# Kernel optimization log

Hardware: AMD Instinct MI355X
Metric: run time of the kernel (lower is better)

## Reference

```python
import jax, jax.numpy as jnp
import numpy as np

N = 3072
E = 32 * N
H = 8
IN_F = 64
OUT_F = 16
ALPHA = 0.2  # LeakyReLU slope
NEG_INF = -9e15


def setup_inputs() -> dict:
    key = jax.random.key(0)
    k1, k2, k3, k4, k5 = jax.random.split(key, 5)
    h = jax.random.normal(k1, (N, IN_F), dtype=jnp.float32)
    edge_index = jax.random.randint(k2, (2, E), 0, N, dtype=jnp.int64)
    S = jax.random.uniform(k3, (N, N), dtype=jnp.float32)
    W = jax.random.normal(k4, (H, IN_F, OUT_F), dtype=jnp.float32) * 0.2
    a = jax.random.normal(k5, (H, 2 * OUT_F, 1), dtype=jnp.float32) * 0.3
    raw_gamma = jnp.ones((H,), dtype=jnp.float32)
    return {"h": h, "edge_index": edge_index, "S": S, "W": W, "a": a, "raw_gamma": raw_gamma}


def reference(h, edge_index, S, W, a, raw_gamma):
    n = h.shape[0]
    # dense adjacency from edge list (to_dense_adj semantics: adj[src, dst] += 1)
    adj = jnp.zeros((n, n), dtype=h.dtype).at[edge_index[0], edge_index[1]].add(1.0)
    # per-head projection: Wh [H, N, O]
    Wh = jnp.einsum('nf,hfo->hno', h, W)
    o = W.shape[2]
    a1 = a[:, :o, 0]  # [H, O]
    a2 = a[:, o:, 0]  # [H, O]
    e1 = jnp.einsum('hno,ho->hn', Wh, a1)  # Wh @ a[:O]
    e2 = jnp.einsum('hno,ho->hn', Wh, a2)  # Wh @ a[O:]
    e = jax.nn.leaky_relu(e1[:, :, None] + e2[:, None, :], ALPHA)  # [H, N, N]
    att = jnp.where(adj[None] > 0, e, jnp.asarray(NEG_INF, e.dtype))
    gamma = jax.nn.softplus(raw_gamma)  # [H], non-negative gate
    att = att * (1.0 + gamma[:, None, None] * S[None])
    att = jax.nn.softmax(att, axis=-1)  # row softmax (dim=1 of [N, N])
    # dropout is identity in eval mode
    h_prime = jnp.einsum('hnm,hmo->hno', att, Wh)  # [H, N, O]
    h_prime = jax.nn.elu(h_prime)  # concat=True per head
    # concat heads along feature dim -> [N, H*O]
    return jnp.transpose(h_prime, (1, 0, 2)).reshape(n, -1)
```

## Files before the change

kernel.cpp:

```cpp
#include <hip/hip_runtime.h>
#include <math.h>

#define N_NODES 3072
#define H_HEADS 8
#define IN_FEAT 64
#define OUT_FEAT 16
#define WORDS_PER_ROW 96
#define MAXD 256
#define SCATTER_BLOCKS 384
#define WH_NPB 16
#define WH_BLOCKS (N_NODES / WH_NPB)

__launch_bounds__(256)
__global__ void scatter_and_wh_kernel(const int* __restrict__ ei, int E,
                                      unsigned int* __restrict__ bits,
                                      const float* __restrict__ hfeat,
                                      const float* __restrict__ W,
                                      const float* __restrict__ a,
                                      float* __restrict__ Wh,
                                      float* __restrict__ e1,
                                      float* __restrict__ e2) {
    __shared__ __align__(16) float Wt[H_HEADS][OUT_FEAT][68];
    __shared__ __align__(16) float hs[WH_NPB][IN_FEAT];

    int tid = threadIdx.x;
    if (blockIdx.x < SCATTER_BLOCKS) {
        int e = blockIdx.x * 256 + tid;
        if (e < E) {
            int r = ei[e];
            int c = ei[E + e];
            atomicOr(&bits[r * WORDS_PER_ROW + (c >> 5)], 1u << (c & 31));
        }
        return;
    }

    int node_base = (blockIdx.x - SCATTER_BLOCKS) * WH_NPB;
    for (int idx = tid; idx < H_HEADS * IN_FEAT * OUT_FEAT; idx += 256) {
        int hh = idx >> 10, f = (idx >> 4) & 63, o = idx & 15;
        Wt[hh][o][f] = W[idx];
    }
    for (int idx = tid; idx < WH_NPB * IN_FEAT; idx += 256)
        hs[idx >> 6][idx & 63] = hfeat[node_base * IN_FEAT + idx];
    __syncthreads();

    int ng = tid >> 7;
    int hh = (tid >> 4) & 7;
    int o  = tid & 15;
    float a1v = a[hh * 2 * OUT_FEAT + o];
    float a2v = a[hh * 2 * OUT_FEAT + OUT_FEAT + o];

    float4 w[16];
#pragma unroll
    for (int q = 0; q < 16; ++q)
        w[q] = *(const float4*)&Wt[hh][o][4 * q];

    for (int n = ng; n < WH_NPB; n += 2) {
        float acc = 0.f;
#pragma unroll
        for (int q = 0; q < 16; ++q) {
            float4 hv = *(const float4*)&hs[n][4 * q];
            acc = fmaf(hv.x, w[q].x, acc);
            acc = fmaf(hv.y, w[q].y, acc);
            acc = fmaf(hv.z, w[q].z, acc);
            acc = fmaf(hv.w, w[q].w, acc);
        }
        int node = node_base + n;
        Wh[(hh * N_NODES + node) * OUT_FEAT + o] = acc;
        float p1 = acc * a1v, p2 = acc * a2v;
#pragma unroll
        for (int m = 1; m < 16; m <<= 1) {
            p1 += __shfl_xor(p1, m, 64);
            p2 += __shfl_xor(p2, m, 64);
        }
        if (o == 0) {
            e1[hh * N_NODES + node] = p1;
            e2[hh * N_NODES + node] = p2;
        }
    }
}

__launch_bounds__(256)
__global__ void gat_main_kernel(const unsigned int* __restrict__ bits,
                                const float* __restrict__ S,
                                const float* __restrict__ Wh,
                                const float* __restrict__ e1,
                                const float* __restrict__ e2,
                                const float* __restrict__ raw_gamma,
                                float* __restrict__ out) {
    __shared__ int lds_j[MAXD];
    __shared__ float lds_s[MAXD];
    __shared__ float lds_p[H_HEADS][MAXD];
    __shared__ int lds_cnt;
    __shared__ int fb_j;
    int i = blockIdx.x;
    int tid = threadIdx.x;
    int wave = tid >> 6, lane = tid & 63;

    if (wave == 0) {
        unsigned int w0 = bits[i * WORDS_PER_ROW + lane];
        unsigned int w1 = (lane < WORDS_PER_ROW - 64) ? bits[i * WORDS_PER_ROW + 64 + lane] : 0u;
        int c = __popc(w0) + __popc(w1);
        int s = c;
#pragma unroll
        for (int d = 1; d < 64; d <<= 1) {
            int v = __shfl_up(s, d, 64);
            if (lane >= d) s += v;
        }
        int off = s - c;
        if (lane == 63) lds_cnt = s;
        unsigned int b = w0;
        int base = lane << 5;
        while (b) {
            int bit = __ffs(b) - 1; b &= b - 1;
            if (off < MAXD) {
                int j = base + bit;
                lds_j[off] = j;
                lds_s[off] = S[i * N_NODES + j];
            }
            ++off;
        }
        b = w1; base = (64 + lane) << 5;
        while (b) {
            int bit = __ffs(b) - 1; b &= b - 1;
            if (off < MAXD) {
                int j = base + bit;
                lds_j[off] = j;
                lds_s[off] = S[i * N_NODES + j];
            }
            ++off;
        }
    }
    __syncthreads();
    int cnt = lds_cnt;
    if (cnt > MAXD) cnt = MAXD;

    if (cnt == 0) {
        if (wave == 0) {
            float bm = 3.4e38f; int bj = 0;
            for (int j = lane; j < N_NODES; j += 64) {
                float sv = S[i * N_NODES + j];
                if (sv < bm) { bm = sv; bj = j; }
            }
            for (int m = 1; m < 64; m <<= 1) {
                float bm2 = __shfl_xor(bm, m, 64);
                int bj2 = __shfl_xor(bj, m, 64);
                if (bm2 < bm || (bm2 == bm && bj2 < bj)) { bm = bm2; bj = bj2; }
            }
            if (lane == 0) fb_j = bj;
        }
        __syncthreads();
        int jj = fb_j;
        if (tid < H_HEADS * OUT_FEAT) {
            int hh = tid >> 4, o = tid & 15;
            float x = Wh[(hh * N_NODES + jj) * OUT_FEAT + o];
            out[i * (H_HEADS * OUT_FEAT) + hh * OUT_FEAT + o] =
                x > 0.f ? x : __expf(x) - 1.f;
        }
        return;
    }

    int half = lane >> 5;
    int hl = lane & 31;
    int hh = wave * 2 + half;
    float g = log1pf(__expf(raw_gamma[hh]));
    float e1v = e1[hh * N_NODES + i];
    float l = 0.f;
    for (int k = hl; k < cnt; k += 32) {
        int j = lds_j[k];
        float x = e1v + e2[hh * N_NODES + j];
        x = x > 0.f ? x : 0.2f * x;
        float p = __expf(x * (1.f + g * lds_s[k]));
        lds_p[hh][k] = p;
        l += p;
    }
#pragma unroll
    for (int m = 1; m < 32; m <<= 1)
        l += __shfl_xor(l, m, 64);

    int kgrp = hl >> 4, o = hl & 15;
    float acc = 0.f;
    for (int kk = kgrp; kk < cnt; kk += 2)
        acc = fmaf(lds_p[hh][kk], Wh[(hh * N_NODES + lds_j[kk]) * OUT_FEAT + o], acc);
    acc += __shfl_xor(acc, 16, 64);
    if (kgrp == 0) {
        float x = acc / l;
        out[i * (H_HEADS * OUT_FEAT) + hh * OUT_FEAT + o] =
            x > 0.f ? x : __expf(x) - 1.f;
    }
}

extern "C" void kernel_launch(void* const* d_in, const int* in_sizes, int n_in,
                              void* d_out, int out_size, void* d_ws, size_t ws_size,
                              hipStream_t stream) {
    const float* hfeat = (const float*)d_in[0];
    const int* ei      = (const int*)d_in[1];
    const float* S     = (const float*)d_in[2];
    const float* W     = (const float*)d_in[3];
    const float* a     = (const float*)d_in[4];
    const float* rg    = (const float*)d_in[5];
    float* out = (float*)d_out;

    char* ws = (char*)d_ws;
    unsigned int* bits = (unsigned int*)ws;
    float* Wh = (float*)(ws + 1179648);
    float* e1 = (float*)(ws + 1179648 + 1572864);
    float* e2 = e1 + H_HEADS * N_NODES;

    int nbits = N_NODES * WORDS_PER_ROW;
    hipMemsetAsync(bits, 0, (size_t)nbits * 4, stream);

    int E = in_sizes[1] / 2;
    scatter_and_wh_kernel<<<SCATTER_BLOCKS + WH_BLOCKS, 256, 0, stream>>>(
        ei, E, bits, hfeat, W, a, Wh, e1, e2);

    gat_main_kernel<<<N_NODES, 256, 0, stream>>>(bits, S, Wh, e1, e2, rg, out);
}
```

Measured before the change: 112.6 us.

## Replace adjacency bitmap with capped per-row neighbor lists and LDS-staged e2

Instead of setting bits in a dense N×N bitmap, the scatter kernel now appends each destination to a per-row list with a capacity of 96, using an atomic counter per row. The main kernel reads these lists directly, so the wave-0 popcount, prefix-scan and bit-extraction pass goes away, and only a 12 KB count array needs clearing instead of a 1.2 MB bitmap. Since lists can hold the same neighbor twice, an O(deg²) check in LDS marks duplicates so they get zero weight. The e1/e2 arrays are stored node-major so each neighbor's eight per-head e2 values load as two float4 and are staged in LDS. The tradeoffs are a silent truncation if any row has more than 96 edges, and a neighbor order that varies between runs.

```diff
diff --git a/kernel.cpp b/kernel.cpp
--- a/kernel.cpp
+++ b/kernel.cpp
@@ -5,21 +5,21 @@
 #define H_HEADS 8
 #define IN_FEAT 64
 #define OUT_FEAT 16
-#define WORDS_PER_ROW 96
-#define MAXD 256
+#define MAXD 96
 #define SCATTER_BLOCKS 384
 #define WH_NPB 16
 #define WH_BLOCKS (N_NODES / WH_NPB)
 
 __launch_bounds__(256)
 __global__ void scatter_and_wh_kernel(const int* __restrict__ ei, int E,
-                                      unsigned int* __restrict__ bits,
+                                      int* __restrict__ cnt,
+                                      int* __restrict__ adj,
                                       const float* __restrict__ hfeat,
                                       const float* __restrict__ W,
                                       const float* __restrict__ a,
                                       float* __restrict__ Wh,
-                                      float* __restrict__ e1,
-                                      float* __restrict__ e2) {
+                                      float* __restrict__ e1t,
+                                      float* __restrict__ e2t) {
     __shared__ __align__(16) float Wt[H_HEADS][OUT_FEAT][68];
     __shared__ __align__(16) float hs[WH_NPB][IN_FEAT];
 
@@ -29,7 +29,8 @@
         if (e < E) {
             int r = ei[e];
             int c = ei[E + e];
-            atomicOr(&bits[r * WORDS_PER_ROW + (c >> 5)], 1u << (c & 31));
+            int pos = atomicAdd(&cnt[r], 1);
+            if (pos < MAXD) adj[r * MAXD + pos] = c;
         }
         return;
     }
@@ -73,66 +74,46 @@
             p2 += __shfl_xor(p2, m, 64);
         }
         if (o == 0) {
-            e1[hh * N_NODES + node] = p1;
-            e2[hh * N_NODES + node] = p2;
+            e1t[node * H_HEADS + hh] = p1;
+            e2t[node * H_HEADS + hh] = p2;
         }
     }
 }
 
 __launch_bounds__(256)
-__global__ void gat_main_kernel(const unsigned int* __restrict__ bits,
+__global__ void gat_main_kernel(const int* __restrict__ cnts,
+                                const int* __restrict__ adj,
                                 const float* __restrict__ S,
                                 const float* __restrict__ Wh,
-                                const float* __restrict__ e1,
-                                const float* __restrict__ e2,
+                                const float* __restrict__ e1t,
+                                const float* __restrict__ e2t,
                                 const float* __restrict__ raw_gamma,
                                 float* __restrict__ out) {
     __shared__ int lds_j[MAXD];
-    __shared__ float lds_s[MAXD];
+    __shared__ float lds_sk[MAXD];
+    __shared__ float lds_keep[MAXD];
+    __shared__ float lds_e2h[H_HEADS][MAXD];
     __shared__ float lds_p[H_HEADS][MAXD];
-    __shared__ int lds_cnt;
     __shared__ int fb_j;
     int i = blockIdx.x;
     int tid = threadIdx.x;
     int wave = tid >> 6, lane = tid & 63;
 
-    if (wave == 0) {
-        unsigned int w0 = bits[i * WORDS_PER_ROW + lane];
-        unsigned int w1 = (lane < WORDS_PER_ROW - 64) ? bits[i * WORDS_PER_ROW + 64 + lane] : 0u;
-        int c = __popc(w0) + __popc(w1);
-        int s = c;
-#pragma unroll
-        for (int d = 1; d < 64; d <<= 1) {
-            int v = __shfl_up(s, d, 64);
-            if (lane >= d) s += v;
-        }
-        int off = s - c;
-        if (lane == 63) lds_cnt = s;
-        unsigned int b = w0;
-        int base = lane << 5;
-        while (b) {
-            int bit = __ffs(b) - 1; b &= b - 1;
-            if (off < MAXD) {
-                int j = base + bit;
-                lds_j[off] = j;
-                lds_s[off] = S[i * N_NODES + j];
-            }
-            ++off;
-        }
-        b = w1; base = (64 + lane) << 5;
-        while (b) {
-            int bit = __ffs(b) - 1; b &= b - 1;
-            if (off < MAXD) {
-                int j = base + bit;
-                lds_j[off] = j;
-                lds_s[off] = S[i * N_NODES + j];
-            }
-            ++off;
-        }
+    int cnt = cnts[i];
+    if (cnt > MAXD) cnt = MAXD;
+
+    if (tid < cnt) {
+        int j = adj[i * MAXD + tid];
+        lds_j[tid] = j;
+        lds_sk[tid] = S[i * N_NODES + j];
+        const float4* ep = (const float4*)&e2t[j * H_HEADS];
+        float4 ea = ep[0], eb = ep[1];
+        lds_e2h[0][tid] = ea.x; lds_e2h[1][tid] = ea.y;
+        lds_e2h[2][tid] = ea.z; lds_e2h[3][tid] = ea.w;
+        lds_e2h[4][tid] = eb.x; lds_e2h[5][tid] = eb.y;
+        lds_e2h[6][tid] = eb.z; lds_e2h[7][tid] = eb.w;
     }
     __syncthreads();
-    int cnt = lds_cnt;
-    if (cnt > MAXD) cnt = MAXD;
 
     if (cnt == 0) {
         if (wave == 0) {
@@ -151,25 +132,33 @@
         __syncthreads();
         int jj = fb_j;
         if (tid < H_HEADS * OUT_FEAT) {
-            int hh = tid >> 4, o = tid & 15;
-            float x = Wh[(hh * N_NODES + jj) * OUT_FEAT + o];
-            out[i * (H_HEADS * OUT_FEAT) + hh * OUT_FEAT + o] =
+            int h2 = tid >> 4, o2 = tid & 15;
+            float x = Wh[(h2 * N_NODES + jj) * OUT_FEAT + o2];
+            out[i * (H_HEADS * OUT_FEAT) + h2 * OUT_FEAT + o2] =
                 x > 0.f ? x : __expf(x) - 1.f;
         }
         return;
     }
+
+    if (tid < cnt) {
+        int j = lds_j[tid];
+        float keep = 1.f;
+        for (int m = 0; m < tid; ++m)
+            if (lds_j[m] == j) keep = 0.f;
+        lds_keep[tid] = keep;
+    }
+    __syncthreads();
 
     int half = lane >> 5;
     int hl = lane & 31;
     int hh = wave * 2 + half;
     float g = log1pf(__expf(raw_gamma[hh]));
-    float e1v = e1[hh * N_NODES + i];
+    float e1v = e1t[i * H_HEADS + hh];
     float l = 0.f;
     for (int k = hl; k < cnt; k += 32) {
-        int j = lds_j[k];
-        float x = e1v + e2[hh * N_NODES + j];
+        float x = e1v + lds_e2h[hh][k];
         x = x > 0.f ? x : 0.2f * x;
-        float p = __expf(x * (1.f + g * lds_s[k]));
+        float p = lds_keep[k] * __expf(x * (1.f + g * lds_sk[k]));
         lds_p[hh][k] = p;
         l += p;
     }
@@ -201,17 +190,17 @@
     float* out = (float*)d_out;
 
     char* ws = (char*)d_ws;
-    unsigned int* bits = (unsigned int*)ws;
-    float* Wh = (float*)(ws + 1179648);
-    float* e1 = (float*)(ws + 1179648 + 1572864);
-    float* e2 = e1 + H_HEADS * N_NODES;
-
-    int nbits = N_NODES * WORDS_PER_ROW;
-    hipMemsetAsync(bits, 0, (size_t)nbits * 4, stream);
+    int* cnt = (int*)ws;
+    int* adj = (int*)(ws + 12288);
+    float* Wh = (float*)(ws + 12288 + 1179648);
+    float* e1t = (float*)(ws + 12288 + 1179648 + 1572864);
+    float* e2t = e1t + N_NODES * H_HEADS;
+
+    hipMemsetAsync(cnt, 0, N_NODES * 4, stream);
 
     int E = in_sizes[1] / 2;
     scatter_and_wh_kernel<<<SCATTER_BLOCKS + WH_BLOCKS, 256, 0, stream>>>(
-        ei, E, bits, hfeat, W, a, Wh, e1, e2);
-
-    gat_main_kernel<<<N_NODES, 256, 0, stream>>>(bits, S, Wh, e1, e2, rg, out);
+        ei, E, cnt, adj, hfeat, W, a, Wh, e1t, e2t);
+
+    gat_main_kernel<<<N_NODES, 256, 0, stream>>>(cnt, adj, S, Wh, e1t, e2t, rg, out);
 }
```

Result: slower. 117.1 us (+4.0%).
